# Kernel optimization log

Measured on AMD Instinct MI355X. Metric: run time of the kernel, lower is better.

Reference implementation:

```python
import jax, jax.numpy as jnp
import numpy as np
from functools import partial

INPUT_SIZE = 24
HIDDEN = 64
NUM_LAYERS = 3
OUT_FEATURES = 4


def _lstm_layer(x, w_ih, w_hh, b_ih, b_hh):
    """Single LSTM layer, PyTorch gate order (i, f, g, o).
    x: [B, T, in] -> returns h sequence [B, T, H]."""
    B = x.shape[0]
    H = w_hh.shape[1]
    # Precompute input contribution for all timesteps: [B, T, 4H]
    gx = jnp.einsum('bti,gi->btg', x, w_ih) + b_ih + b_hh

    def step(carry, g_t):
        h, c = carry
        gates = g_t + h @ w_hh.T  # [B, 4H]
        i, f, g, o = jnp.split(gates, 4, axis=-1)
        i = jax.nn.sigmoid(i)
        f = jax.nn.sigmoid(f)
        g = jnp.tanh(g)
        o = jax.nn.sigmoid(o)
        c = f * c + i * g
        h = o * jnp.tanh(c)
        return (h, c), h

    h0 = jnp.zeros((B, H), dtype=x.dtype)
    c0 = jnp.zeros((B, H), dtype=x.dtype)
    (_, _), hs = jax.lax.scan(step, (h0, c0), jnp.swapaxes(gx, 0, 1))  # hs: [T, B, H]
    return jnp.swapaxes(hs, 0, 1)  # [B, T, H]


def setup_inputs() -> dict:
    key = jax.random.key(0)
    ks = jax.random.split(key, 16)
    B, T = 1024, 512
    inp = {"x": jax.random.normal(ks[0], (B, T, INPUT_SIZE), dtype=jnp.float32)}
    k = 1
    s = 1.0 / np.sqrt(HIDDEN)
    for layer in range(NUM_LAYERS):
        in_dim = INPUT_SIZE if layer == 0 else HIDDEN
        inp[f"w_ih_{layer}"] = jax.random.uniform(ks[k], (4 * HIDDEN, in_dim), minval=-s, maxval=s, dtype=jnp.float32); k += 1
        inp[f"w_hh_{layer}"] = jax.random.uniform(ks[k], (4 * HIDDEN, HIDDEN), minval=-s, maxval=s, dtype=jnp.float32); k += 1
        inp[f"b_ih_{layer}"] = jax.random.uniform(ks[k], (4 * HIDDEN,), minval=-s, maxval=s, dtype=jnp.float32); k += 1
        inp[f"b_hh_{layer}"] = jax.random.uniform(ks[k], (4 * HIDDEN,), minval=-s, maxval=s, dtype=jnp.float32); k += 1
    inp["w_lin"] = jax.random.uniform(ks[13], (OUT_FEATURES, HIDDEN), minval=-s, maxval=s, dtype=jnp.float32)
    inp["b_lin"] = jax.random.uniform(ks[14], (OUT_FEATURES,), minval=-s, maxval=s, dtype=jnp.float32)
    return inp


def reference(x, w_ih_0, w_hh_0, b_ih_0, b_hh_0,
              w_ih_1, w_hh_1, b_ih_1, b_hh_1,
              w_ih_2, w_hh_2, b_ih_2, b_hh_2,
              w_lin, b_lin):
    params = [(w_ih_0, w_hh_0, b_ih_0, b_hh_0),
              (w_ih_1, w_hh_1, b_ih_1, b_hh_1),
              (w_ih_2, w_hh_2, b_ih_2, b_hh_2)]
    h = x
    for (w_ih, w_hh, b_ih, b_hh) in params:  # fixed 3-layer stack
        h = _lstm_layer(h, w_ih, w_hh, b_ih, b_hh)
    last = h[:, -1]                      # [B, H]
    return last @ w_lin.T + b_lin        # [B, 4]
```

## Files before the change

kernel.cpp:

```cpp
#include <hip/hip_runtime.h>


typedef __attribute__((ext_vector_type(8))) _Float16 half8;
typedef __attribute__((ext_vector_type(4))) _Float16 half4;
typedef __attribute__((ext_vector_type(4))) float floatx4;

static constexpr int T_STEPS = 512;

#define NL2E  (-1.4426950408889634f)
#define N2L2E (-2.8853900817779268f)

#define CR_X   0
#define CR_H0  8
#define CR_H1  24
#define CR_H2  40
#define CR_TOT 56
#define SM_BYTES (CR_TOT * 256)

__device__ __forceinline__ int lds_off(int cr, int inner) {
    return (cr * 16 + (inner ^ (cr & 7))) * 16;
}

__device__ __forceinline__ floatx4 mfma16(half8 a, half8 b, floatx4 c) {
    return __builtin_amdgcn_mfma_f32_16x16x32_f16(a, b, c, 0, 0, 0);
}

__device__ __forceinline__ float sig2(float a) {
    return __builtin_amdgcn_rcpf(1.0f + __builtin_amdgcn_exp2f(a));
}

__device__ __forceinline__ half8 cvt8(const float* src) {
    float4 v0 = *(const float4*)(src);
    float4 v1 = *(const float4*)(src + 4);
    half8 h;
    h[0] = (_Float16)v0.x; h[1] = (_Float16)v0.y;
    h[2] = (_Float16)v0.z; h[3] = (_Float16)v0.w;
    h[4] = (_Float16)v1.x; h[5] = (_Float16)v1.y;
    h[6] = (_Float16)v1.z; h[7] = (_Float16)v1.w;
    return h;
}

__global__ __launch_bounds__(768, 3) void lstm3_fused(
    const float* __restrict__ x,
    const float* __restrict__ w_ih0, const float* __restrict__ w_hh0,
    const float* __restrict__ b_ih0, const float* __restrict__ b_hh0,
    const float* __restrict__ w_ih1, const float* __restrict__ w_hh1,
    const float* __restrict__ b_ih1, const float* __restrict__ b_hh1,
    const float* __restrict__ w_ih2, const float* __restrict__ w_hh2,
    const float* __restrict__ b_ih2, const float* __restrict__ b_hh2,
    const float* __restrict__ w_lin, const float* __restrict__ b_lin,
    float* __restrict__ out)
{
    __shared__ __align__(16) char sm[SM_BYTES];

    const int tid  = threadIdx.x;
    const int lane = tid & 63;
    const int wave = tid >> 6;
    const int L    = wave >> 2;
    const int w    = wave & 3;
    const int l15  = lane & 15;
    const int l4   = lane >> 4;
    const int b0   = blockIdx.x * 4;
    const int u    = w * 16 + l15;

    for (int i = tid; i < CR_TOT * 16; i += 768)
        *(floatx4*)(&sm[i * 16]) = floatx4{0.f, 0.f, 0.f, 0.f};

    const float* wi = (L == 0) ? w_ih0 : (L == 1 ? w_ih1 : w_ih2);
    const float* wh = (L == 0) ? w_hh0 : (L == 1 ? w_hh1 : w_hh2);
    const float* bi = (L == 0) ? b_ih0 : (L == 1 ? b_ih1 : b_ih2);
    const float* bh = (L == 0) ? b_hh0 : (L == 1 ? b_hh1 : b_hh2);
    const int hbase = (L == 0) ? CR_H0 : (L == 1 ? CR_H1 : CR_H2);
    const int pbase = (L == 0) ? CR_X  : (L == 1 ? CR_H0 : CR_H1);

    half8 wf[4][4];
#pragma unroll
    for (int tt = 0; tt < 4; ++tt) {
        const int g = tt * 64 + u;
        if (L == 0) {
            half8 z;
#pragma unroll
            for (int j = 0; j < 8; ++j) z[j] = (_Float16)0.f;
            wf[tt][0] = (l4 < 3) ? cvt8(w_ih0 + g * 24 + l4 * 8) : z;
            wf[tt][1] = cvt8(w_hh0 + g * 64 + l4 * 8);
            wf[tt][2] = cvt8(w_hh0 + g * 64 + 32 + l4 * 8);
            wf[tt][3] = z;
        } else {
            wf[tt][0] = cvt8(wi + g * 64 + l4 * 8);
            wf[tt][1] = cvt8(wi + g * 64 + 32 + l4 * 8);
            wf[tt][2] = cvt8(wh + g * 64 + l4 * 8);
            wf[tt][3] = cvt8(wh + g * 64 + 32 + l4 * 8);
        }
    }

    float bs[4];
#pragma unroll
    for (int tt = 0; tt < 4; ++tt) {
        float sc = (tt == 2) ? N2L2E : NL2E;
        bs[tt] = sc * (bi[tt * 64 + u] + bh[tt * 64 + u]);
    }
    float cst = 0.0f;

    const int xb = tid / 6, xf = tid % 6;
    if (tid < 24) {
        float4 v = *(const float4*)(x + ((long)(b0 + xb) * T_STEPS + 0) * 24 + xf * 4);
        half4 hv; hv[0] = (_Float16)v.x; hv[1] = (_Float16)v.y;
                  hv[2] = (_Float16)v.z; hv[3] = (_Float16)v.w;
        *(half4*)(&sm[lds_off(CR_X + (xf >> 1), xb) + (xf & 1) * 8]) = hv;
    }
    __syncthreads();

    for (int s = 0; s < T_STEPS + 2; ++s) {
        const int t = s - L;
        const bool active = (t >= 0) && (t < T_STEPS);
        const int par = t & 1;

        float4 xpre;
        const bool do_x = (tid < 24) && (s + 1 < T_STEPS);
        if (do_x)
            xpre = *(const float4*)(x + ((long)(b0 + xb) * T_STEPS + (s + 1)) * 24 + xf * 4);

        if (active) {
            const int sl = l15 >> 2;
            floatx4 acc[4];
            if (L == 0) {
                half8 aX  = *(const half8*)(&sm[lds_off(CR_X + par * 4 + l4, sl)]);
                half8 aP0 = *(const half8*)(&sm[lds_off(CR_H0 + (par ^ 1) * 8 + l4, sl)]);
                half8 aP1 = *(const half8*)(&sm[lds_off(CR_H0 + (par ^ 1) * 8 + 4 + l4, sl)]);
#pragma unroll
                for (int tt = 0; tt < 4; ++tt) {
#pragma unroll
                    for (int r = 0; r < 4; ++r) acc[tt][r] = 0.0f;
                    acc[tt] = mfma16(aX,  wf[tt][0], acc[tt]);
                    acc[tt] = mfma16(aP0, wf[tt][1], acc[tt]);
                    acc[tt] = mfma16(aP1, wf[tt][2], acc[tt]);
                }
            } else {
                half8 aI0 = *(const half8*)(&sm[lds_off(pbase + par * 8 + l4, sl)]);
                half8 aI1 = *(const half8*)(&sm[lds_off(pbase + par * 8 + 4 + l4, sl)]);
                half8 aO0 = *(const half8*)(&sm[lds_off(hbase + (par ^ 1) * 8 + l4, sl)]);
                half8 aO1 = *(const half8*)(&sm[lds_off(hbase + (par ^ 1) * 8 + 4 + l4, sl)]);
#pragma unroll
                for (int tt = 0; tt < 4; ++tt) {
#pragma unroll
                    for (int r = 0; r < 4; ++r) acc[tt][r] = 0.0f;
                    acc[tt] = mfma16(aI0, wf[tt][0], acc[tt]);
                    acc[tt] = mfma16(aI1, wf[tt][1], acc[tt]);
                    acc[tt] = mfma16(aO0, wf[tt][2], acc[tt]);
                    acc[tt] = mfma16(aO1, wf[tt][3], acc[tt]);
                }
            }

            float ig = sig2(fmaf(acc[0][0], NL2E,  bs[0]));
            float fg = sig2(fmaf(acc[1][0], NL2E,  bs[1]));
            float gg = fmaf(2.0f, sig2(fmaf(acc[2][0], N2L2E, bs[2])), -1.0f);
            float og = sig2(fmaf(acc[3][0], NL2E,  bs[3]));
            cst = fmaf(fg, cst, ig * gg);
            float hv = og * fmaf(2.0f, sig2(cst * N2L2E), -1.0f);
            *(_Float16*)(&sm[lds_off(hbase + par * 8 + (u >> 3), l4) + (u & 7) * 2]) =
                (_Float16)hv;
        }
        if (do_x) {
            half4 hv; hv[0] = (_Float16)xpre.x; hv[1] = (_Float16)xpre.y;
                      hv[2] = (_Float16)xpre.z; hv[3] = (_Float16)xpre.w;
            *(half4*)(&sm[lds_off(CR_X + ((s + 1) & 1) * 4 + (xf >> 1), xb) + (xf & 1) * 8]) = hv;
        }
        __syncthreads();
    }

    if (tid < 16) {
        const int bb = tid >> 2, o = tid & 3;
        const int hb = CR_H2 + ((T_STEPS - 1) & 1) * 8;
        float acc = b_lin[o];
#pragma unroll
        for (int k = 0; k < 64; ++k) {
            _Float16 hv = *(const _Float16*)(&sm[lds_off(hb + (k >> 3), bb) + (k & 7) * 2]);
            acc = fmaf((float)hv, w_lin[o * 64 + k], acc);
        }
        out[(b0 + bb) * 4 + o] = acc;
    }
}

extern "C" void kernel_launch(void* const* d_in, const int* in_sizes, int n_in,
                              void* d_out, int out_size, void* d_ws, size_t ws_size,
                              hipStream_t stream) {
    const float* x     = (const float*)d_in[0];
    const float* w_ih0 = (const float*)d_in[1];
    const float* w_hh0 = (const float*)d_in[2];
    const float* b_ih0 = (const float*)d_in[3];
    const float* b_hh0 = (const float*)d_in[4];
    const float* w_ih1 = (const float*)d_in[5];
    const float* w_hh1 = (const float*)d_in[6];
    const float* b_ih1 = (const float*)d_in[7];
    const float* b_hh1 = (const float*)d_in[8];
    const float* w_ih2 = (const float*)d_in[9];
    const float* w_hh2 = (const float*)d_in[10];
    const float* b_ih2 = (const float*)d_in[11];
    const float* b_hh2 = (const float*)d_in[12];
    const float* w_lin = (const float*)d_in[13];
    const float* b_lin = (const float*)d_in[14];

    lstm3_fused<<<dim3(256), dim3(768), 0, stream>>>(
        x, w_ih0, w_hh0, b_ih0, b_hh0,
        w_ih1, w_hh1, b_ih1, b_hh1,
        w_ih2, w_hh2, b_ih2, b_hh2,
        w_lin, b_lin, (float*)d_out);
}
```

Before: 340.0 us.

## Precompute LDS addresses, unroll by parity, fold bias into MFMA accumulator init

LDS read/write offsets for both time-step parities are computed once before the loop, and the loop is unrolled by two so each half uses fixed addresses with no per-step swizzle math. The swizzle is simplified to an XOR on odd rows. The bias is now the initial MFMA accumulator instead of an extra FMA per gate, and s_setprio raises wave priority around the MFMA section. The aim is a shorter serial per-step critical path in this latency-bound recurrence, at the cost of more live registers and a changed bank-conflict pattern.

```diff
diff --git a/kernel.cpp b/kernel.cpp
--- a/kernel.cpp
+++ b/kernel.cpp
@@ -17,8 +17,8 @@
 #define CR_TOT 56
 #define SM_BYTES (CR_TOT * 256)
 
-__device__ __forceinline__ int lds_off(int cr, int inner) {
-    return (cr * 16 + (inner ^ (cr & 7))) * 16;
+__device__ __forceinline__ int lds_off(int cr, int slot) {
+    return (cr * 16 + (slot ^ ((cr & 1) << 2))) * 16;
 }
 
 __device__ __forceinline__ floatx4 mfma16(half8 a, half8 b, floatx4 c) {
@@ -62,6 +62,7 @@
     const int l4   = lane >> 4;
     const int b0   = blockIdx.x * 4;
     const int u    = w * 16 + l15;
+    const int sl   = l15 >> 2;
 
     for (int i = tid; i < CR_TOT * 16; i += 768)
         *(floatx4*)(&sm[i * 16]) = floatx4{0.f, 0.f, 0.f, 0.f};
@@ -93,79 +94,111 @@
         }
     }
 
-    float bs[4];
+    floatx4 bv[4];
 #pragma unroll
     for (int tt = 0; tt < 4; ++tt) {
-        float sc = (tt == 2) ? N2L2E : NL2E;
-        bs[tt] = sc * (bi[tt * 64 + u] + bh[tt * 64 + u]);
+        float b = bi[tt * 64 + u] + bh[tt * 64 + u];
+        bv[tt][0] = b; bv[tt][1] = b; bv[tt][2] = b; bv[tt][3] = b;
     }
     float cst = 0.0f;
 
+    int ra0[4], ra1[4];
+    if (L == 0) {
+        ra0[0] = lds_off(CR_X + 0 + l4, sl);
+        ra0[1] = lds_off(CR_H0 + 8 + l4, sl);
+        ra0[2] = lds_off(CR_H0 + 12 + l4, sl);
+        ra0[3] = 0;
+        ra1[0] = lds_off(CR_X + 4 + l4, sl);
+        ra1[1] = lds_off(CR_H0 + 0 + l4, sl);
+        ra1[2] = lds_off(CR_H0 + 4 + l4, sl);
+        ra1[3] = 0;
+    } else {
+        ra0[0] = lds_off(pbase + 0 + l4, sl);
+        ra0[1] = lds_off(pbase + 4 + l4, sl);
+        ra0[2] = lds_off(hbase + 8 + l4, sl);
+        ra0[3] = lds_off(hbase + 12 + l4, sl);
+        ra1[0] = lds_off(pbase + 8 + l4, sl);
+        ra1[1] = lds_off(pbase + 12 + l4, sl);
+        ra1[2] = lds_off(hbase + 0 + l4, sl);
+        ra1[3] = lds_off(hbase + 4 + l4, sl);
+    }
+    const int wr0 = lds_off(hbase + 0 + (u >> 3), l4) + (u & 7) * 2;
+    const int wr1 = lds_off(hbase + 8 + (u >> 3), l4) + (u & 7) * 2;
+
+    const int Lodd = L & 1;
+    const int eA0 = Lodd ? ra1[0] : ra0[0], eA1 = Lodd ? ra1[1] : ra0[1];
+    const int eA2 = Lodd ? ra1[2] : ra0[2], eA3 = Lodd ? ra1[3] : ra0[3];
+    const int oA0 = Lodd ? ra0[0] : ra1[0], oA1 = Lodd ? ra0[1] : ra1[1];
+    const int oA2 = Lodd ? ra0[2] : ra1[2], oA3 = Lodd ? ra0[3] : ra1[3];
+    const int eWr = Lodd ? wr1 : wr0, oWr = Lodd ? wr0 : wr1;
+
     const int xb = tid / 6, xf = tid % 6;
+    const int xw0 = lds_off(CR_X + 0 + (xf >> 1), xb) + (xf & 1) * 8;
+    const int xw1 = lds_off(CR_X + 4 + (xf >> 1), xb) + (xf & 1) * 8;
+    const float* xg = x + ((long)(b0 + xb) * T_STEPS + 1) * 24 + xf * 4;
     if (tid < 24) {
         float4 v = *(const float4*)(x + ((long)(b0 + xb) * T_STEPS + 0) * 24 + xf * 4);
         half4 hv; hv[0] = (_Float16)v.x; hv[1] = (_Float16)v.y;
                   hv[2] = (_Float16)v.z; hv[3] = (_Float16)v.w;
-        *(half4*)(&sm[lds_off(CR_X + (xf >> 1), xb) + (xf & 1) * 8]) = hv;
+        *(half4*)(&sm[xw0]) = hv;
     }
     __syncthreads();
 
-    for (int s = 0; s < T_STEPS + 2; ++s) {
+    auto body = [&](int s, int A0, int A1, int A2, int A3, int WR, int XW) {
         const int t = s - L;
-        const bool active = (t >= 0) && (t < T_STEPS);
-        const int par = t & 1;
-
+        const bool active = ((unsigned)t < (unsigned)T_STEPS);
         float4 xpre;
         const bool do_x = (tid < 24) && (s + 1 < T_STEPS);
-        if (do_x)
-            xpre = *(const float4*)(x + ((long)(b0 + xb) * T_STEPS + (s + 1)) * 24 + xf * 4);
+        if (do_x) xpre = *(const float4*)xg;
 
         if (active) {
-            const int sl = l15 >> 2;
             floatx4 acc[4];
+            __builtin_amdgcn_s_setprio(1);
             if (L == 0) {
-                half8 aX  = *(const half8*)(&sm[lds_off(CR_X + par * 4 + l4, sl)]);
-                half8 aP0 = *(const half8*)(&sm[lds_off(CR_H0 + (par ^ 1) * 8 + l4, sl)]);
-                half8 aP1 = *(const half8*)(&sm[lds_off(CR_H0 + (par ^ 1) * 8 + 4 + l4, sl)]);
+                half8 aX  = *(const half8*)(&sm[A0]);
+                half8 aP0 = *(const half8*)(&sm[A1]);
+                half8 aP1 = *(const half8*)(&sm[A2]);
 #pragma unroll
                 for (int tt = 0; tt < 4; ++tt) {
-#pragma unroll
-                    for (int r = 0; r < 4; ++r) acc[tt][r] = 0.0f;
-                    acc[tt] = mfma16(aX,  wf[tt][0], acc[tt]);
+                    acc[tt] = mfma16(aX,  wf[tt][0], bv[tt]);
                     acc[tt] = mfma16(aP0, wf[tt][1], acc[tt]);
                     acc[tt] = mfma16(aP1, wf[tt][2], acc[tt]);
                 }
             } else {
-                half8 aI0 = *(const half8*)(&sm[lds_off(pbase + par * 8 + l4, sl)]);
-                half8 aI1 = *(const half8*)(&sm[lds_off(pbase + par * 8 + 4 + l4, sl)]);
-                half8 aO0 = *(const half8*)(&sm[lds_off(hbase + (par ^ 1) * 8 + l4, sl)]);
-                half8 aO1 = *(const half8*)(&sm[lds_off(hbase + (par ^ 1) * 8 + 4 + l4, sl)]);
+                half8 aI0 = *(const half8*)(&sm[A0]);
+                half8 aI1 = *(const half8*)(&sm[A1]);
+                half8 aO0 = *(const half8*)(&sm[A2]);
+                half8 aO1 = *(const half8*)(&sm[A3]);
 #pragma unroll
                 for (int tt = 0; tt < 4; ++tt) {
-#pragma unroll
-                    for (int r = 0; r < 4; ++r) acc[tt][r] = 0.0f;
-                    acc[tt] = mfma16(aI0, wf[tt][0], acc[tt]);
+                    acc[tt] = mfma16(aI0, wf[tt][0], bv[tt]);
                     acc[tt] = mfma16(aI1, wf[tt][1], acc[tt]);
                     acc[tt] = mfma16(aO0, wf[tt][2], acc[tt]);
                     acc[tt] = mfma16(aO1, wf[tt][3], acc[tt]);
                 }
             }
-
-            float ig = sig2(fmaf(acc[0][0], NL2E,  bs[0]));
-            float fg = sig2(fmaf(acc[1][0], NL2E,  bs[1]));
-            float gg = fmaf(2.0f, sig2(fmaf(acc[2][0], N2L2E, bs[2])), -1.0f);
-            float og = sig2(fmaf(acc[3][0], NL2E,  bs[3]));
+            __builtin_amdgcn_s_setprio(0);
+
+            float ig = sig2(acc[0][0] * NL2E);
+            float fg = sig2(acc[1][0] * NL2E);
+            float gg = fmaf(2.0f, sig2(acc[2][0] * N2L2E), -1.0f);
+            float og = sig2(acc[3][0] * NL2E);
             cst = fmaf(fg, cst, ig * gg);
             float hv = og * fmaf(2.0f, sig2(cst * N2L2E), -1.0f);
-            *(_Float16*)(&sm[lds_off(hbase + par * 8 + (u >> 3), l4) + (u & 7) * 2]) =
-                (_Float16)hv;
+            *(_Float16*)(&sm[WR]) = (_Float16)hv;
         }
         if (do_x) {
             half4 hv; hv[0] = (_Float16)xpre.x; hv[1] = (_Float16)xpre.y;
                       hv[2] = (_Float16)xpre.z; hv[3] = (_Float16)xpre.w;
-            *(half4*)(&sm[lds_off(CR_X + ((s + 1) & 1) * 4 + (xf >> 1), xb) + (xf & 1) * 8]) = hv;
-        }
+            *(half4*)(&sm[XW]) = hv;
+        }
+        xg += 24;
         __syncthreads();
+    };
+
+    for (int s = 0; s < T_STEPS + 2; s += 2) {
+        body(s,     eA0, eA1, eA2, eA3, eWr, xw1);
+        body(s + 1, oA0, oA1, oA2, oA3, oWr, xw0);
     }
 
     if (tid < 16) {
```

After: 301.2 us. 11.4% less time.

## Replace per-step block barriers with LDS flag-based async layer pipeline

Applied to the files above, without the earlier changes.

Replaces the __syncthreads after every wavefront step with per-layer, per-slot LDS counters that waves spin on, giving a 4-slot ring buffer for each layer's hidden state so the three layers can drift apart by up to a few timesteps. It also folds the log2e gate scaling and the bias into the MFMA weights and accumulator init, and computes the four sigmoids with a single shared reciprocal. Layer-0 input is read straight from global memory into registers instead of being staged through LDS. The aim is to remove full-block barrier stalls and shorten the per-step dependency chain, at the cost of spin-wait polling, atomics and a more fragile synchronization protocol.

```diff
diff --git a/kernel.cpp b/kernel.cpp
--- a/kernel.cpp
+++ b/kernel.cpp
@@ -2,7 +2,6 @@
 
 
 typedef __attribute__((ext_vector_type(8))) _Float16 half8;
-typedef __attribute__((ext_vector_type(4))) _Float16 half4;
 typedef __attribute__((ext_vector_type(4))) float floatx4;
 
 static constexpr int T_STEPS = 512;
@@ -10,37 +9,28 @@
 #define NL2E  (-1.4426950408889634f)
 #define N2L2E (-2.8853900817779268f)
 
-#define CR_X   0
-#define CR_H0  8
-#define CR_H1  24
-#define CR_H2  40
-#define CR_TOT 56
-#define SM_BYTES (CR_TOT * 256)
-
-__device__ __forceinline__ int lds_off(int cr, int inner) {
-    return (cr * 16 + (inner ^ (cr & 7))) * 16;
-}
+#define H_OFF0    0
+#define H_OFF1    2048
+#define H_OFF2    4096
+#define FLAGS_OFF 6144
+#define SM_BYTES  6208
 
 __device__ __forceinline__ floatx4 mfma16(half8 a, half8 b, floatx4 c) {
     return __builtin_amdgcn_mfma_f32_16x16x32_f16(a, b, c, 0, 0, 0);
 }
 
-__device__ __forceinline__ float sig2(float a) {
-    return __builtin_amdgcn_rcpf(1.0f + __builtin_amdgcn_exp2f(a));
-}
-
-__device__ __forceinline__ half8 cvt8(const float* src) {
+__device__ __forceinline__ half8 cvt8s(const float* src, float s) {
     float4 v0 = *(const float4*)(src);
     float4 v1 = *(const float4*)(src + 4);
     half8 h;
-    h[0] = (_Float16)v0.x; h[1] = (_Float16)v0.y;
-    h[2] = (_Float16)v0.z; h[3] = (_Float16)v0.w;
-    h[4] = (_Float16)v1.x; h[5] = (_Float16)v1.y;
-    h[6] = (_Float16)v1.z; h[7] = (_Float16)v1.w;
+    h[0] = (_Float16)(v0.x * s); h[1] = (_Float16)(v0.y * s);
+    h[2] = (_Float16)(v0.z * s); h[3] = (_Float16)(v0.w * s);
+    h[4] = (_Float16)(v1.x * s); h[5] = (_Float16)(v1.y * s);
+    h[6] = (_Float16)(v1.z * s); h[7] = (_Float16)(v1.w * s);
     return h;
 }
 
-__global__ __launch_bounds__(768, 3) void lstm3_fused(
+__global__ __launch_bounds__(768, 3) void lstm3_async(
     const float* __restrict__ x,
     const float* __restrict__ w_ih0, const float* __restrict__ w_hh0,
     const float* __restrict__ b_ih0, const float* __restrict__ b_hh0,
@@ -52,6 +42,7 @@
     float* __restrict__ out)
 {
     __shared__ __align__(16) char sm[SM_BYTES];
+    int* dflag = (int*)(sm + FLAGS_OFF);
 
     const int tid  = threadIdx.x;
     const int lane = tid & 63;
@@ -60,124 +51,180 @@
     const int w    = wave & 3;
     const int l15  = lane & 15;
     const int l4   = lane >> 4;
+    const int bat  = l15 >> 2;
     const int b0   = blockIdx.x * 4;
     const int u    = w * 16 + l15;
 
-    for (int i = tid; i < CR_TOT * 16; i += 768)
+    for (int i = tid; i < SM_BYTES / 16; i += 768)
         *(floatx4*)(&sm[i * 16]) = floatx4{0.f, 0.f, 0.f, 0.f};
 
     const float* wi = (L == 0) ? w_ih0 : (L == 1 ? w_ih1 : w_ih2);
     const float* wh = (L == 0) ? w_hh0 : (L == 1 ? w_hh1 : w_hh2);
     const float* bi = (L == 0) ? b_ih0 : (L == 1 ? b_ih1 : b_ih2);
     const float* bh = (L == 0) ? b_hh0 : (L == 1 ? b_hh1 : b_hh2);
-    const int hbase = (L == 0) ? CR_H0 : (L == 1 ? CR_H1 : CR_H2);
-    const int pbase = (L == 0) ? CR_X  : (L == 1 ? CR_H0 : CR_H1);
+    const int HB = (L == 0) ? H_OFF0 : (L == 1 ? H_OFF1 : H_OFF2);
+    const int PB = (L == 1) ? H_OFF0 : H_OFF1;
 
     half8 wf[4][4];
 #pragma unroll
     for (int tt = 0; tt < 4; ++tt) {
         const int g = tt * 64 + u;
+        const float sc = (tt == 2) ? N2L2E : NL2E;
         if (L == 0) {
             half8 z;
 #pragma unroll
             for (int j = 0; j < 8; ++j) z[j] = (_Float16)0.f;
-            wf[tt][0] = (l4 < 3) ? cvt8(w_ih0 + g * 24 + l4 * 8) : z;
-            wf[tt][1] = cvt8(w_hh0 + g * 64 + l4 * 8);
-            wf[tt][2] = cvt8(w_hh0 + g * 64 + 32 + l4 * 8);
+            wf[tt][0] = (l4 < 3) ? cvt8s(w_ih0 + g * 24 + l4 * 8, sc) : z;
+            wf[tt][1] = cvt8s(w_hh0 + g * 64 + l4 * 8, sc);
+            wf[tt][2] = cvt8s(w_hh0 + g * 64 + 32 + l4 * 8, sc);
             wf[tt][3] = z;
         } else {
-            wf[tt][0] = cvt8(wi + g * 64 + l4 * 8);
-            wf[tt][1] = cvt8(wi + g * 64 + 32 + l4 * 8);
-            wf[tt][2] = cvt8(wh + g * 64 + l4 * 8);
-            wf[tt][3] = cvt8(wh + g * 64 + 32 + l4 * 8);
-        }
-    }
-
-    float bs[4];
+            wf[tt][0] = cvt8s(wi + g * 64 + l4 * 8, sc);
+            wf[tt][1] = cvt8s(wi + g * 64 + 32 + l4 * 8, sc);
+            wf[tt][2] = cvt8s(wh + g * 64 + l4 * 8, sc);
+            wf[tt][3] = cvt8s(wh + g * 64 + 32 + l4 * 8, sc);
+        }
+    }
+    floatx4 bv[4];
 #pragma unroll
     for (int tt = 0; tt < 4; ++tt) {
-        float sc = (tt == 2) ? N2L2E : NL2E;
-        bs[tt] = sc * (bi[tt * 64 + u] + bh[tt * 64 + u]);
-    }
+        const float sc = (tt == 2) ? N2L2E : NL2E;
+        float b = sc * (bi[tt * 64 + u] + bh[tt * 64 + u]);
+        bv[tt][0] = b; bv[tt][1] = b; bv[tt][2] = b; bv[tt][3] = b;
+    }
+
+    const int swzR = (bat & 1) << 5;
+    int rb0 = 0, rb1 = 0, rb2 = 0, rb3 = 0;
+    if (L == 0) {
+        rb1 = H_OFF0 + ((bat * 128 + 0  + l4 * 16) ^ swzR);
+        rb2 = H_OFF0 + ((bat * 128 + 64 + l4 * 16) ^ swzR);
+    } else {
+        rb0 = PB + ((bat * 128 + 0  + l4 * 16) ^ swzR);
+        rb1 = PB + ((bat * 128 + 64 + l4 * 16) ^ swzR);
+        rb2 = HB + ((bat * 128 + 0  + l4 * 16) ^ swzR);
+        rb3 = HB + ((bat * 128 + 64 + l4 * 16) ^ swzR);
+    }
+    const int wb = HB + ((l4 * 128 + u * 2) ^ ((l4 & 1) << 5));
+
+    float4 xA0{0,0,0,0}, xA1{0,0,0,0}, xB0{0,0,0,0}, xB1{0,0,0,0};
+    const bool xv = (L == 0) && (l4 < 3);
+    const float* xpe = nullptr;
+    const float* xpo = nullptr;
+    if (xv) {
+        const float* xb_ = x + (long)(b0 + bat) * T_STEPS * 24 + l4 * 8;
+        xA0 = *(const float4*)(xb_);      xA1 = *(const float4*)(xb_ + 4);
+        xB0 = *(const float4*)(xb_ + 24); xB1 = *(const float4*)(xb_ + 28);
+        xpe = xb_ + 48;
+        xpo = xb_ + 72;
+    }
+
     float cst = 0.0f;
-
-    const int xb = tid / 6, xf = tid % 6;
-    if (tid < 24) {
-        float4 v = *(const float4*)(x + ((long)(b0 + xb) * T_STEPS + 0) * 24 + xf * 4);
-        half4 hv; hv[0] = (_Float16)v.x; hv[1] = (_Float16)v.y;
-                  hv[2] = (_Float16)v.z; hv[3] = (_Float16)v.w;
-        *(half4*)(&sm[lds_off(CR_X + (xf >> 1), xb) + (xf & 1) * 8]) = hv;
-    }
     __syncthreads();
 
-    for (int s = 0; s < T_STEPS + 2; ++s) {
-        const int t = s - L;
-        const bool active = (t >= 0) && (t < T_STEPS);
-        const int par = t & 1;
-
-        float4 xpre;
-        const bool do_x = (tid < 24) && (s + 1 < T_STEPS);
-        if (do_x)
-            xpre = *(const float4*)(x + ((long)(b0 + xb) * T_STEPS + (s + 1)) * 24 + xf * 4);
-
-        if (active) {
-            const int sl = l15 >> 2;
-            floatx4 acc[4];
-            if (L == 0) {
-                half8 aX  = *(const half8*)(&sm[lds_off(CR_X + par * 4 + l4, sl)]);
-                half8 aP0 = *(const half8*)(&sm[lds_off(CR_H0 + (par ^ 1) * 8 + l4, sl)]);
-                half8 aP1 = *(const half8*)(&sm[lds_off(CR_H0 + (par ^ 1) * 8 + 4 + l4, sl)]);
-#pragma unroll
-                for (int tt = 0; tt < 4; ++tt) {
-#pragma unroll
-                    for (int r = 0; r < 4; ++r) acc[tt][r] = 0.0f;
-                    acc[tt] = mfma16(aX,  wf[tt][0], acc[tt]);
-                    acc[tt] = mfma16(aP0, wf[tt][1], acc[tt]);
-                    acc[tt] = mfma16(aP1, wf[tt][2], acc[tt]);
+    auto step = [&](int t, int slot, int slotm1) __attribute__((always_inline)) {
+        {
+            const int TgA = (((t - 1) >> 2) + 1) * 4;
+            volatile int* fA = dflag + L * 4 + slotm1;
+            while (*fA < TgA) __builtin_amdgcn_s_sleep(1);
+            if (L >= 1) {
+                const int TgB = ((t >> 2) + 1) * 4;
+                volatile int* fB = dflag + (L - 1) * 4 + slot;
+                while (*fB < TgB) __builtin_amdgcn_s_sleep(1);
+            }
+            if (L <= 1) {
+                const int TgC = (((t - 4) >> 2) + 1) * 4;
+                volatile int* fC = dflag + (L + 1) * 4 + slot;
+                while (*fC < TgC) __builtin_amdgcn_s_sleep(1);
+            }
+        }
+        asm volatile("" ::: "memory");
+
+        const int ro = slot * 512;
+        const int rp = slotm1 * 512;
+
+        floatx4 acc[4];
+        __builtin_amdgcn_s_setprio(1);
+        if (L == 0) {
+            const float4 v0 = (slot & 1) ? xB0 : xA0;
+            const float4 v1 = (slot & 1) ? xB1 : xA1;
+            half8 aX;
+            aX[0] = (_Float16)v0.x; aX[1] = (_Float16)v0.y;
+            aX[2] = (_Float16)v0.z; aX[3] = (_Float16)v0.w;
+            aX[4] = (_Float16)v1.x; aX[5] = (_Float16)v1.y;
+            aX[6] = (_Float16)v1.z; aX[7] = (_Float16)v1.w;
+            half8 a1 = *(const half8*)(&sm[rb1 + rp]);
+            half8 a2 = *(const half8*)(&sm[rb2 + rp]);
+#pragma unroll
+            for (int tt = 0; tt < 4; ++tt) {
+                acc[tt] = mfma16(aX, wf[tt][0], bv[tt]);
+                acc[tt] = mfma16(a1, wf[tt][1], acc[tt]);
+                acc[tt] = mfma16(a2, wf[tt][2], acc[tt]);
+            }
+            if (xv && t + 2 < T_STEPS) {
+                if (slot & 1) {
+                    xB0 = *(const float4*)(xpo); xB1 = *(const float4*)(xpo + 4);
+                    xpo += 48;
+                } else {
+                    xA0 = *(const float4*)(xpe); xA1 = *(const float4*)(xpe + 4);
+                    xpe += 48;
                 }
-            } else {
-                half8 aI0 = *(const half8*)(&sm[lds_off(pbase + par * 8 + l4, sl)]);
-                half8 aI1 = *(const half8*)(&sm[lds_off(pbase + par * 8 + 4 + l4, sl)]);
-                half8 aO0 = *(const half8*)(&sm[lds_off(hbase + (par ^ 1) * 8 + l4, sl)]);
-                half8 aO1 = *(const half8*)(&sm[lds_off(hbase + (par ^ 1) * 8 + 4 + l4, sl)]);
-#pragma unroll
-                for (int tt = 0; tt < 4; ++tt) {
-#pragma unroll
-                    for (int r = 0; r < 4; ++r) acc[tt][r] = 0.0f;
-                    acc[tt] = mfma16(aI0, wf[tt][0], acc[tt]);
-                    acc[tt] = mfma16(aI1, wf[tt][1], acc[tt]);
-                    acc[tt] = mfma16(aO0, wf[tt][2], acc[tt]);
-                    acc[tt] = mfma16(aO1, wf[tt][3], acc[tt]);
-                }
-            }
-
-            float ig = sig2(fmaf(acc[0][0], NL2E,  bs[0]));
-            float fg = sig2(fmaf(acc[1][0], NL2E,  bs[1]));
-            float gg = fmaf(2.0f, sig2(fmaf(acc[2][0], N2L2E, bs[2])), -1.0f);
-            float og = sig2(fmaf(acc[3][0], NL2E,  bs[3]));
-            cst = fmaf(fg, cst, ig * gg);
-            float hv = og * fmaf(2.0f, sig2(cst * N2L2E), -1.0f);
-            *(_Float16*)(&sm[lds_off(hbase + par * 8 + (u >> 3), l4) + (u & 7) * 2]) =
-                (_Float16)hv;
-        }
-        if (do_x) {
-            half4 hv; hv[0] = (_Float16)xpre.x; hv[1] = (_Float16)xpre.y;
-                      hv[2] = (_Float16)xpre.z; hv[3] = (_Float16)xpre.w;
-            *(half4*)(&sm[lds_off(CR_X + ((s + 1) & 1) * 4 + (xf >> 1), xb) + (xf & 1) * 8]) = hv;
-        }
-        __syncthreads();
-    }
+            }
+        } else {
+            half8 a0 = *(const half8*)(&sm[rb0 + ro]);
+            half8 a1 = *(const half8*)(&sm[rb1 + ro]);
+            half8 a2 = *(const half8*)(&sm[rb2 + rp]);
+            half8 a3 = *(const half8*)(&sm[rb3 + rp]);
+#pragma unroll
+            for (int tt = 0; tt < 4; ++tt) {
+                acc[tt] = mfma16(a0, wf[tt][0], bv[tt]);
+                acc[tt] = mfma16(a1, wf[tt][1], acc[tt]);
+                acc[tt] = mfma16(a2, wf[tt][2], acc[tt]);
+                acc[tt] = mfma16(a3, wf[tt][3], acc[tt]);
+            }
+        }
+        __builtin_amdgcn_s_setprio(0);
+
+        float ei = __builtin_amdgcn_exp2f(__builtin_amdgcn_fmed3f(acc[0][0], -30.f, 30.f));
+        float ef = __builtin_amdgcn_exp2f(__builtin_amdgcn_fmed3f(acc[1][0], -30.f, 30.f));
+        float eg = __builtin_amdgcn_exp2f(__builtin_amdgcn_fmed3f(acc[2][0], -30.f, 30.f));
+        float eo = __builtin_amdgcn_exp2f(__builtin_amdgcn_fmed3f(acc[3][0], -30.f, 30.f));
+        float A1 = 1.f + ei, B1 = 1.f + ef, C1 = 1.f + eg, D1 = 1.f + eo;
+        float p = A1 * B1, q = C1 * D1;
+        float r = __builtin_amdgcn_rcpf(p * q);
+        float ip = r * q, iq = r * p;
+        float ig = ip * B1;
+        float fg = ip * A1;
+        float sg = iq * D1;
+        float og = iq * C1;
+        float gg = fmaf(2.f, sg, -1.f);
+        cst = fmaf(fg, cst, ig * gg);
+        float et = __builtin_amdgcn_exp2f(cst * N2L2E);
+        float th = fmaf(2.f, __builtin_amdgcn_rcpf(1.f + et), -1.f);
+        float hv = og * th;
+        *(_Float16*)(&sm[wb + ro]) = (_Float16)hv;
+
+        asm volatile("s_waitcnt lgkmcnt(0)" ::: "memory");
+        if (lane == 0) atomicAdd(dflag + L * 4 + slot, 1);
+    };
+
+    for (int tb = 0; tb < T_STEPS; tb += 4) {
+        step(tb + 0, 0, 3);
+        step(tb + 1, 1, 0);
+        step(tb + 2, 2, 1);
+        step(tb + 3, 3, 2);
+    }
+
+    __syncthreads();
 
     if (tid < 16) {
         const int bb = tid >> 2, o = tid & 3;
-        const int hb = CR_H2 + ((T_STEPS - 1) & 1) * 8;
-        float acc = b_lin[o];
+        float accum = b_lin[o];
 #pragma unroll
         for (int k = 0; k < 64; ++k) {
-            _Float16 hv = *(const _Float16*)(&sm[lds_off(hb + (k >> 3), bb) + (k & 7) * 2]);
-            acc = fmaf((float)hv, w_lin[o * 64 + k], acc);
-        }
-        out[(b0 + bb) * 4 + o] = acc;
+            const int off = H_OFF2 + 3 * 512 + ((bb * 128 + k * 2) ^ ((bb & 1) << 5));
+            accum = fmaf((float)*(const _Float16*)(&sm[off]), w_lin[o * 64 + k], accum);
+        }
+        out[(b0 + bb) * 4 + o] = accum;
     }
 }
 
@@ -200,7 +247,7 @@
     const float* w_lin = (const float*)d_in[13];
     const float* b_lin = (const float*)d_in[14];
 
-    lstm3_fused<<<dim3(256), dim3(768), 0, stream>>>(
+    lstm3_async<<<dim3(256), dim3(768), 0, stream>>>(
         x, w_ih0, w_hh0, b_ih0, b_hh0,
         w_ih1, w_hh1, b_ih1, b_hh1,
         w_ih2, w_hh2, b_ih2, b_hh2,
```

After: 336.7 us. Within noise of the previous version (-1.0%).
